# Optimization experiments

Measured on AMD Instinct MI355X. Metric: run time of the kernel, lower is better.

The kernel has to match this reference:

```python
import jax, jax.numpy as jnp
import numpy as np

B, S, H = 4, 2048, 1024
DECAY_RATE = 0.5  # MemoryModule decay: exp(-decay_rate * k), k=1 (most recent pattern)


def setup_inputs() -> dict:
    key = jax.random.key(0)
    ks = jax.random.split(key, 7)
    hidden_states = jax.random.normal(ks[0], (B, S, H), dtype=jnp.float32)
    # past attention pattern: valid row-stochastic attention probs [B, S, S]
    pa = jax.random.uniform(ks[1], (B, S, S), dtype=jnp.float32)
    past_attention = pa / pa.sum(-1, keepdims=True)
    scale = 1.0 / np.sqrt(H).astype(np.float32)
    Wq = jax.random.normal(ks[2], (H, H), dtype=jnp.float32) * scale
    Wk = jax.random.normal(ks[3], (H, H), dtype=jnp.float32) * scale
    Wv = jax.random.normal(ks[4], (H, H), dtype=jnp.float32) * scale
    Wm = jax.random.normal(ks[5], (H, H), dtype=jnp.float32) * scale
    w_gate = jax.random.normal(ks[6], (H,), dtype=jnp.float32) * scale
    return {"hidden_states": hidden_states, "past_attention": past_attention,
            "Wq": Wq, "Wk": Wk, "Wv": Wv, "Wm": Wm, "w_gate": w_gate}


def reference(hidden_states, past_attention, Wq, Wk, Wv, Wm, w_gate):
    h = hidden_states.shape[-1]
    inv_sqrt_h = 1.0 / (h ** 0.5)
    # QKV projections (hidden -> hidden)
    q = jnp.einsum('bsh,hd->bsd', hidden_states, Wq)
    k = jnp.einsum('bsh,hd->bsd', hidden_states, Wk)
    v = jnp.einsum('bsh,hd->bsd', hidden_states, Wv)
    # base attention scores QK^T / sqrt(H)
    scores = jnp.einsum('bqd,bkd->bqk', q, k) * inv_sqrt_h
    # --- memory bias ---
    # decayed history pattern (single most-recent entry, k=1)
    memory = past_attention * jnp.exp(jnp.float32(-DECAY_RATE * 1.0))  # [B,S,S]
    # per-token scalar gate from query
    gates = jax.nn.sigmoid(jnp.einsum('bsh,h->bs', q, w_gate))  # [B,S]
    memory_values = jnp.einsum('bqk,bkd->bqd', memory, v)        # memory @ V
    transformed = jnp.einsum('bsh,hd->bsd', memory_values, Wm)   # memory_transform (no bias)
    gated_memory = gates[..., None] * transformed
    memory_bias = jnp.einsum('bqd,bkd->bqk', gated_memory, k) * inv_sqrt_h
    # augmented attention
    probs = jax.nn.softmax(scores + memory_bias, axis=-1)
    context = jnp.einsum('bqk,bkd->bqd', probs, v)
    return context
```

## Files before the change

kernel.cpp:

```cpp
#include <hip/hip_runtime.h>
#include <hip/hip_bf16.h>

typedef __attribute__((ext_vector_type(4))) float f32x4;
typedef __attribute__((ext_vector_type(8))) __bf16 bf16x8;

__device__ __forceinline__ unsigned short f2bf(float f) {
    union { float f; unsigned u; } x; x.f = f;
    unsigned r = x.u + 0x7fffu + ((x.u >> 16) & 1u);
    return (unsigned short)(r >> 16);
}
__device__ __forceinline__ float bf2f(unsigned short b) {
    union { unsigned u; float f; } x; x.u = ((unsigned)b) << 16;
    return x.f;
}

__device__ __forceinline__ void gload16(const void* g, void* l) {
    __builtin_amdgcn_global_load_lds(
        (const __attribute__((address_space(1))) unsigned int*)g,
        (__attribute__((address_space(3))) unsigned int*)l,
        16, 0, 0);
}

template <int N> __device__ __forceinline__ void vm_wait();
template <> __device__ __forceinline__ void vm_wait<0>() { asm volatile("s_waitcnt vmcnt(0)" ::: "memory"); }
template <> __device__ __forceinline__ void vm_wait<2>() { asm volatile("s_waitcnt vmcnt(2)" ::: "memory"); }
template <> __device__ __forceinline__ void vm_wait<4>() { asm volatile("s_waitcnt vmcnt(4)" ::: "memory"); }

__global__ __launch_bounds__(256) void k_prep(
    const float* __restrict__ hs, const float* __restrict__ pa,
    const float* __restrict__ Wq, const float* __restrict__ Wk,
    const float* __restrict__ Wv, const float* __restrict__ Wm,
    unsigned short* __restrict__ hs_bf, unsigned short* __restrict__ pa_bf,
    unsigned short* __restrict__ WT, float decay) {
    __shared__ float tile[32][33];
    unsigned b = blockIdx.x;
    int t = threadIdx.x;
    if (b < 16384u) {
        int i = b * 256 + t;
        float4 v = reinterpret_cast<const float4*>(pa)[i];
        union { unsigned short u[4]; uint2 q; } o;
        o.u[0] = f2bf(v.x * decay); o.u[1] = f2bf(v.y * decay);
        o.u[2] = f2bf(v.z * decay); o.u[3] = f2bf(v.w * decay);
        reinterpret_cast<uint2*>(pa_bf)[i] = o.q;
    } else if (b < 24576u) {
        int i = (b - 16384u) * 256 + t;
        float4 v = reinterpret_cast<const float4*>(hs)[i];
        union { unsigned short u[4]; uint2 q; } o;
        o.u[0] = f2bf(v.x); o.u[1] = f2bf(v.y);
        o.u[2] = f2bf(v.z); o.u[3] = f2bf(v.w);
        reinterpret_cast<uint2*>(hs_bf)[i] = o.q;
    } else {
        unsigned bb = b - 24576u;
        int z = bb >> 10, rem = bb & 1023;
        int bx = rem & 31, by = rem >> 5;
        const float* src = z == 0 ? Wq : z == 1 ? Wk : z == 2 ? Wv : Wm;
        unsigned short* dst = WT + (size_t)z * 1024 * 1024;
        int lx = t & 31, ly8 = t >> 5;
        int x = bx * 32 + lx;
#pragma unroll
        for (int i = 0; i < 4; i++)
            tile[ly8 + i * 8][lx] = src[(size_t)(by * 32 + ly8 + i * 8) * 1024 + x];
        __syncthreads();
        int tx = by * 32 + lx;
#pragma unroll
        for (int i = 0; i < 4; i++)
            dst[(size_t)(bx * 32 + ly8 + i * 8) * 1024 + tx] = f2bf(tile[lx][ly8 + i * 8]);
    }
}

__global__ __launch_bounds__(256) void k_post(
    const unsigned short* __restrict__ C3, unsigned short* __restrict__ v_t,
    const float* __restrict__ wg, float* __restrict__ gates) {
    __shared__ unsigned short tile[32][33];
    unsigned b = blockIdx.x;
    int t = threadIdx.x;
    if (b < 8192u) {
        int bx = b & 31, by = (b >> 5) & 63, bz = b >> 11;
        int lx = t & 31, ly8 = t >> 5;
        int x = bx * 32 + lx;
#pragma unroll
        for (int i = 0; i < 4; i++) {
            int y = by * 32 + ly8 + i * 8;
            tile[ly8 + i * 8][lx] = C3[(size_t)(bz * 2048 + y) * 3072 + 2048 + x];
        }
        __syncthreads();
        int tx = by * 32 + lx;
#pragma unroll
        for (int i = 0; i < 4; i++) {
            int ty = bx * 32 + ly8 + i * 8;
            v_t[(size_t)bz * 1024 * 2048 + (size_t)ty * 2048 + tx] = tile[lx][ly8 + i * 8];
        }
    } else {
        unsigned bb = b - 8192u;
        int lane = t & 63;
        int row = bb * 4 + (t >> 6);
        const unsigned short* qr = C3 + (size_t)row * 3072 + lane * 16;
        uint4 a0 = *reinterpret_cast<const uint4*>(qr);
        uint4 a1 = *reinterpret_cast<const uint4*>(qr + 8);
        const float* wp = wg + lane * 16;
        float s = 0.f;
        unsigned ua[8] = {a0.x, a0.y, a0.z, a0.w, a1.x, a1.y, a1.z, a1.w};
#pragma unroll
        for (int j = 0; j < 8; j++) {
            s += bf2f((unsigned short)(ua[j] & 0xffff)) * wp[2 * j];
            s += bf2f((unsigned short)(ua[j] >> 16)) * wp[2 * j + 1];
        }
#pragma unroll
        for (int o = 1; o < 64; o <<= 1) s += __shfl_xor(s, o);
        if (lane == 0) gates[row] = 1.f / (1.f + __expf(-s));
    }
}

__global__ __launch_bounds__(256) void k_softmax(const float* __restrict__ logits,
                                                 unsigned short* __restrict__ probs) {
    __shared__ float red[8];
    size_t base = (size_t)blockIdx.x * 2048;
    const float4* src = reinterpret_cast<const float4*>(logits + base);
    int t = threadIdx.x;
    int wave = t >> 6, lane = t & 63;
    float4 v0 = src[t], v1 = src[t + 256];
    float m = fmaxf(fmaxf(fmaxf(v0.x, v0.y), fmaxf(v0.z, v0.w)),
                    fmaxf(fmaxf(v1.x, v1.y), fmaxf(v1.z, v1.w)));
#pragma unroll
    for (int o = 1; o < 64; o <<= 1) m = fmaxf(m, __shfl_xor(m, o));
    if (lane == 0) red[wave] = m;
    __syncthreads();
    m = fmaxf(fmaxf(red[0], red[1]), fmaxf(red[2], red[3]));
    float e[8];
    e[0] = __expf(v0.x - m); e[1] = __expf(v0.y - m);
    e[2] = __expf(v0.z - m); e[3] = __expf(v0.w - m);
    e[4] = __expf(v1.x - m); e[5] = __expf(v1.y - m);
    e[6] = __expf(v1.z - m); e[7] = __expf(v1.w - m);
    float s = e[0] + e[1] + e[2] + e[3] + e[4] + e[5] + e[6] + e[7];
#pragma unroll
    for (int o = 1; o < 64; o <<= 1) s += __shfl_xor(s, o);
    if (lane == 0) red[4 + wave] = s;
    __syncthreads();
    s = red[4] + red[5] + red[6] + red[7];
    float inv = 1.f / s;
    union { unsigned short u[4]; uint2 q; } o0, o1;
#pragma unroll
    for (int j = 0; j < 4; j++) o0.u[j] = f2bf(e[j] * inv);
#pragma unroll
    for (int j = 0; j < 4; j++) o1.u[j] = f2bf(e[4 + j] * inv);
    reinterpret_cast<uint2*>(probs + base)[t] = o0.q;
    reinterpret_cast<uint2*>(probs + base)[t + 256] = o1.q;
}

template <int BN>
struct Geo {
    static constexpr int WN = BN / 64;
    static constexpr int WM = 8 / WN;
    static constexpr int WROWS = 256 / WM;
    static constexpr int MF = WROWS / 16;
    static constexpr int MP = MF / 4;
    static constexpr int ASZ = 256 * 64 * 2;
    static constexpr int BSZ = BN * 64 * 2;
    static constexpr int BUFSZ = ASZ + BSZ;
};

#define GPH(BUFOFF, MB, LB, STG, VMW)                                                   \
    {                                                                                   \
        const char* aB = smem + (BUFOFF);                                               \
        const char* bB = aB + G::ASZ;                                                   \
        bf16x8 af[G::MP * 2];                                                           \
        _Pragma("unroll") for (int mm = 0; mm < G::MP; ++mm)                            \
        _Pragma("unroll") for (int kk = 0; kk < 2; ++kk) {                              \
            int rowx = wrow + ((MB) + mm) * 16 + fr;                                    \
            int slot = (kk * 4 + kq) ^ (rowx & 7);                                      \
            af[mm * 2 + kk] = *reinterpret_cast<const bf16x8*>(aB + rowx * 128 + slot * 16); \
        }                                                                               \
        if (LB) {                                                                       \
            _Pragma("unroll") for (int nn = 0; nn < 4; ++nn)                            \
            _Pragma("unroll") for (int kk = 0; kk < 2; ++kk) {                          \
                int rowx = wcol + nn * 16 + fr;                                         \
                int slot = (kk * 4 + kq) ^ (rowx & 7);                                  \
                bfrag[nn * 2 + kk] = *reinterpret_cast<const bf16x8*>(bB + rowx * 128 + slot * 16); \
            }                                                                           \
        }                                                                               \
        STG;                                                                            \
        __builtin_amdgcn_sched_barrier(0);                                              \
        VMW;                                                                            \
        __builtin_amdgcn_s_barrier();                                                   \
        asm volatile("s_waitcnt lgkmcnt(0)" ::: "memory");                              \
        __builtin_amdgcn_sched_barrier(0);                                              \
        __builtin_amdgcn_s_setprio(1);                                                  \
        _Pragma("unroll") for (int mm = 0; mm < G::MP; ++mm)                            \
        _Pragma("unroll") for (int nn = 0; nn < 4; ++nn)                                \
        _Pragma("unroll") for (int kk = 0; kk < 2; ++kk)                                \
            acc[(MB) + mm][nn] = __builtin_amdgcn_mfma_f32_16x16x32_bf16(               \
                af[mm * 2 + kk], bfrag[nn * 2 + kk], acc[(MB) + mm][nn], 0, 0, 0);      \
        __builtin_amdgcn_s_setprio(0);                                                  \
        __builtin_amdgcn_sched_barrier(0);                                              \
        __builtin_amdgcn_s_barrier();                                                   \
        __builtin_amdgcn_sched_barrier(0);                                              \
    }

template <int EPI, int BN>
__global__ __launch_bounds__(512, 2) void k_gemm8(
    const unsigned short* __restrict__ A, int ldA, long long bsA,
    const unsigned short* __restrict__ Bt, int ldB, long long bsB,
    void* __restrict__ Cv, int ldC, long long bsC,
    const unsigned short* __restrict__ Qm, int ldQ,
    const float* __restrict__ gates, float alpha, int K,
    int NX, int NY, int NB, int yf) {
    using G = Geo<BN>;
    extern __shared__ char smem[];
    const int NT = K >> 6, NI = K >> 7;

    unsigned b = blockIdx.x;
    unsigned wg = (b & 7) * (gridDim.x >> 3) + (b >> 3);
    int xT, yT, zB;
    if (yf) {
        yT = wg % NY; unsigned r2 = wg / NY;
        xT = r2 % NX; zB = (int)(r2 / NX) % NB;
    } else {
        xT = wg % NX; unsigned r2 = wg / NX;
        yT = r2 % NY; zB = (int)(r2 / NY) % NB;
    }

    const unsigned short* Ab = A + (size_t)zB * (size_t)bsA;
    const unsigned short* Bb = Bt + (size_t)zB * (size_t)bsB;

    int t = threadIdx.x, lane = t & 63, wave = t >> 6;
    int wc = wave % G::WN, wr = wave / G::WN;
    int fr = lane & 15, kq = lane >> 4;
    int wrow = wr * G::WROWS, wcol = wc * 64;
    int trow = t >> 3, csx = (t & 7) ^ (trow & 7);
    long long rowTile = (long long)yT * 256, colTile = (long long)xT * BN;

    f32x4 acc[G::MF][4];
#pragma unroll
    for (int m = 0; m < G::MF; ++m)
#pragma unroll
        for (int n = 0; n < 4; ++n) acc[m][n] = (f32x4){0.f, 0.f, 0.f, 0.f};
    bf16x8 bfrag[8];

    auto stageA = [&](int buf, int h, int tt) {
        int kt = tt < NT ? tt : NT - 1;
#pragma unroll
        for (int rr = 0; rr < 2; ++rr) {
            const unsigned short* src =
                Ab + (size_t)(rowTile + h * 128 + rr * 64 + trow) * (size_t)ldA + kt * 64 + csx * 8;
            gload16(src, smem + buf * G::BUFSZ + h * 16384 + rr * 8192 + t * 16);
        }
    };
    auto stageB = [&](int buf, int h, int tt) {
        int kt = tt < NT ? tt : NT - 1;
        if (BN == 256) {
#pragma unroll
            for (int rr = 0; rr < 2; ++rr) {
                const unsigned short* src =
                    Bb + (size_t)(colTile + h * 128 + rr * 64 + trow) * (size_t)ldB + kt * 64 + csx * 8;
                gload16(src, smem + buf * G::BUFSZ + G::ASZ + h * 16384 + rr * 8192 + t * 16);
            }
        } else {
            const unsigned short* src =
                Bb + (size_t)(colTile + h * 64 + trow) * (size_t)ldB + kt * 64 + csx * 8;
            gload16(src, smem + buf * G::BUFSZ + G::ASZ + h * 8192 + t * 16);
        }
    };

    stageA(0, 0, 0); stageA(0, 1, 0);
    stageB(0, 0, 0); stageB(0, 1, 0);
    stageB(1, 0, 1); stageB(1, 1, 1);
    __builtin_amdgcn_sched_barrier(0);
    vm_wait<0>();
    __builtin_amdgcn_s_barrier();
    __builtin_amdgcn_sched_barrier(0);

    constexpr int VMN = (BN == 256) ? 4 : 2;
    for (int i = 0; i < NI; ++i) {
        int t1 = 2 * i + 1, t2 = 2 * i + 2, t3 = 2 * i + 3;
        GPH(0,          0,         1, stageA(1, 0, t1), (void)0);
        GPH(0,          G::MP,     0, stageA(1, 1, t1), (void)0);
        GPH(0,          2 * G::MP, 0, stageB(0, 0, t2), (void)0);
        GPH(0,          3 * G::MP, 0, stageB(0, 1, t2), vm_wait<VMN>());
        GPH(G::BUFSZ,   0,         1, stageA(0, 0, t2), (void)0);
        GPH(G::BUFSZ,   G::MP,     0, stageA(0, 1, t2), (void)0);
        GPH(G::BUFSZ,   2 * G::MP, 0, stageB(1, 0, t3), (void)0);
        GPH(G::BUFSZ,   3 * G::MP, 0, stageB(1, 1, t3), vm_wait<VMN>());
    }
    vm_wait<0>();

    long long rb0 = rowTile + wrow + kq * 4;
    long long cb0 = colTile + wcol + fr;
    if (EPI == 0) {
        unsigned short* C = (unsigned short*)Cv + (size_t)zB * (size_t)bsC;
#pragma unroll
        for (int m = 0; m < G::MF; ++m)
#pragma unroll
            for (int n = 0; n < 4; ++n)
#pragma unroll
                for (int r = 0; r < 4; ++r)
                    C[(size_t)(rb0 + m * 16 + r) * (size_t)ldC + cb0 + n * 16] =
                        f2bf(acc[m][n][r] * alpha);
    } else if (EPI == 1) {
        unsigned short* C = (unsigned short*)Cv;
#pragma unroll
        for (int m = 0; m < G::MF; ++m)
#pragma unroll
            for (int r = 0; r < 4; ++r) {
                long long row = rb0 + m * 16 + r;
                float g = gates[row];
#pragma unroll
                for (int n = 0; n < 4; ++n) {
                    long long col = cb0 + n * 16;
                    float v = (bf2f(Qm[(size_t)row * (size_t)ldQ + col]) + g * acc[m][n][r]) * alpha;
                    C[(size_t)row * (size_t)ldC + col] = f2bf(v);
                }
            }
    } else {
        float* C = (float*)Cv + (size_t)zB * (size_t)bsC;
#pragma unroll
        for (int m = 0; m < G::MF; ++m)
#pragma unroll
            for (int n = 0; n < 4; ++n)
#pragma unroll
                for (int r = 0; r < 4; ++r)
                    C[(size_t)(rb0 + m * 16 + r) * (size_t)ldC + cb0 + n * 16] =
                        acc[m][n][r] * alpha;
    }
}

extern "C" void kernel_launch(void* const* d_in, const int* in_sizes, int n_in,
                              void* d_out, int out_size, void* d_ws, size_t ws_size,
                              hipStream_t stream) {
    const float* hs = (const float*)d_in[0];
    const float* pa = (const float*)d_in[1];
    const float* Wq = (const float*)d_in[2];
    const float* Wk = (const float*)d_in[3];
    const float* Wv = (const float*)d_in[4];
    const float* Wm = (const float*)d_in[5];
    const float* wg = (const float*)d_in[6];
    float* out = (float*)d_out;

    const int B = 4, S = 2048, H = 1024;
    const size_t BS = (size_t)B * S;
    const size_t BSH = BS * H;
    const size_t BSS = (size_t)B * S * S;
    const float inv_sqrt_h = 0.03125f;
    const float decay = 0.60653065971263342f;

    char* ws = (char*)d_ws;
    size_t off = 0;
    auto take = [&](size_t bytes) {
        char* p = ws + off;
        off += (bytes + 255) & ~(size_t)255;
        return p;
    };
    unsigned short* hs_bf = (unsigned short*)take(BSH * 2);
    unsigned short* WT    = (unsigned short*)take(4ull * H * H * 2);
    float* gates          = (float*)take(BS * 4);
    unsigned short* C3    = (unsigned short*)take(BS * 3 * H * 2);
    unsigned short* v_t   = (unsigned short*)take(BSH * 2);
    unsigned short* pa_bf = (unsigned short*)take(BSS * 2);
    float* logits         = (float*)take(BSS * 4);
    unsigned short* mv    = (unsigned short*)d_out;
    unsigned short* u_bf  = hs_bf;
    unsigned short* probs = pa_bf;
    unsigned short* WmT   = WT + 3ull * H * H;

    (void)hipFuncSetAttribute((const void*)k_gemm8<0, 128>, hipFuncAttributeMaxDynamicSharedMemorySize, 98304);
    (void)hipFuncSetAttribute((const void*)k_gemm8<1, 128>, hipFuncAttributeMaxDynamicSharedMemorySize, 98304);
    (void)hipFuncSetAttribute((const void*)k_gemm8<2, 128>, hipFuncAttributeMaxDynamicSharedMemorySize, 98304);
    (void)hipFuncSetAttribute((const void*)k_gemm8<2, 256>, hipFuncAttributeMaxDynamicSharedMemorySize, 131072);

    k_prep<<<dim3(28672), 256, 0, stream>>>(hs, pa, Wq, Wk, Wv, Wm, hs_bf, pa_bf, WT, decay);
    k_gemm8<0, 128><<<768, 512, 98304, stream>>>(
        hs_bf, H, 0, WT, H, 0, C3, 3 * H, 0, nullptr, 0, nullptr, 1.f, H, 24, 32, 1, 0);
    k_post<<<dim3(10240), 256, 0, stream>>>(C3, v_t, wg, gates);
    k_gemm8<0, 128><<<256, 512, 98304, stream>>>(
        pa_bf, S, (long long)S * S, v_t, S, (long long)H * S, mv, H, (long long)S * H,
        nullptr, 0, nullptr, 1.f, S, 8, 8, 4, 1);
    k_gemm8<1, 128><<<256, 512, 98304, stream>>>(
        mv, H, 0, WmT, H, 0, u_bf, H, 0, C3, 3 * H, gates, inv_sqrt_h, H, 8, 32, 1, 0);
    k_gemm8<2, 256><<<256, 512, 131072, stream>>>(
        u_bf, H, (long long)S * H, C3 + H, 3 * H, (long long)S * 3 * H,
        logits, S, (long long)S * S, nullptr, 0, nullptr, 1.f, H, 8, 8, 4, 1);
    k_softmax<<<dim3((unsigned)BS), 256, 0, stream>>>(logits, probs);
    k_gemm8<2, 128><<<256, 512, 98304, stream>>>(
        probs, S, (long long)S * S, v_t, S, (long long)H * S, out, H, (long long)S * H,
        nullptr, 0, nullptr, 1.f, S, 8, 8, 4, 1);
}
```

Measured before the change: 267.3 us.

## Switch GEMMs to 256x256 tiles with BK=32 and 4-stage LDS pipeline

Replaces the templated BN=128/256 GEMM with a single 256x256 tile kernel that uses K-step 32, a 4-buffer ring of LDS stages with three tiles of prefetch in flight, and a new swizzle for 64-byte rows. The aim is to hide global-load latency better and raise arithmetic intensity per block. The cost is halving grid sizes for several GEMMs (as few as 128 blocks on a 256-CU part), which leaves the GPU underoccupied. It also means twice as many barrier phases per unit of K.

```diff
diff --git a/kernel.cpp b/kernel.cpp
--- a/kernel.cpp
+++ b/kernel.cpp
@@ -23,8 +23,7 @@
 
 template <int N> __device__ __forceinline__ void vm_wait();
 template <> __device__ __forceinline__ void vm_wait<0>() { asm volatile("s_waitcnt vmcnt(0)" ::: "memory"); }
-template <> __device__ __forceinline__ void vm_wait<2>() { asm volatile("s_waitcnt vmcnt(2)" ::: "memory"); }
-template <> __device__ __forceinline__ void vm_wait<4>() { asm volatile("s_waitcnt vmcnt(4)" ::: "memory"); }
+template <> __device__ __forceinline__ void vm_wait<8>() { asm volatile("s_waitcnt vmcnt(8)" ::: "memory"); }
 
 __global__ __launch_bounds__(256) void k_prep(
     const float* __restrict__ hs, const float* __restrict__ pa,
@@ -147,66 +146,50 @@
     reinterpret_cast<uint2*>(probs + base)[t + 256] = o1.q;
 }
 
-template <int BN>
-struct Geo {
-    static constexpr int WN = BN / 64;
-    static constexpr int WM = 8 / WN;
-    static constexpr int WROWS = 256 / WM;
-    static constexpr int MF = WROWS / 16;
-    static constexpr int MP = MF / 4;
-    static constexpr int ASZ = 256 * 64 * 2;
-    static constexpr int BSZ = BN * 64 * 2;
-    static constexpr int BUFSZ = ASZ + BSZ;
-};
-
-#define GPH(BUFOFF, MB, LB, STG, VMW)                                                   \
-    {                                                                                   \
-        const char* aB = smem + (BUFOFF);                                               \
-        const char* bB = aB + G::ASZ;                                                   \
-        bf16x8 af[G::MP * 2];                                                           \
-        _Pragma("unroll") for (int mm = 0; mm < G::MP; ++mm)                            \
-        _Pragma("unroll") for (int kk = 0; kk < 2; ++kk) {                              \
-            int rowx = wrow + ((MB) + mm) * 16 + fr;                                    \
-            int slot = (kk * 4 + kq) ^ (rowx & 7);                                      \
-            af[mm * 2 + kk] = *reinterpret_cast<const bf16x8*>(aB + rowx * 128 + slot * 16); \
-        }                                                                               \
-        if (LB) {                                                                       \
-            _Pragma("unroll") for (int nn = 0; nn < 4; ++nn)                            \
-            _Pragma("unroll") for (int kk = 0; kk < 2; ++kk) {                          \
-                int rowx = wcol + nn * 16 + fr;                                         \
-                int slot = (kk * 4 + kq) ^ (rowx & 7);                                  \
-                bfrag[nn * 2 + kk] = *reinterpret_cast<const bf16x8*>(bB + rowx * 128 + slot * 16); \
-            }                                                                           \
-        }                                                                               \
-        STG;                                                                            \
-        __builtin_amdgcn_sched_barrier(0);                                              \
-        VMW;                                                                            \
-        __builtin_amdgcn_s_barrier();                                                   \
-        asm volatile("s_waitcnt lgkmcnt(0)" ::: "memory");                              \
-        __builtin_amdgcn_sched_barrier(0);                                              \
-        __builtin_amdgcn_s_setprio(1);                                                  \
-        _Pragma("unroll") for (int mm = 0; mm < G::MP; ++mm)                            \
-        _Pragma("unroll") for (int nn = 0; nn < 4; ++nn)                                \
-        _Pragma("unroll") for (int kk = 0; kk < 2; ++kk)                                \
-            acc[(MB) + mm][nn] = __builtin_amdgcn_mfma_f32_16x16x32_bf16(               \
-                af[mm * 2 + kk], bfrag[nn * 2 + kk], acc[(MB) + mm][nn], 0, 0, 0);      \
-        __builtin_amdgcn_s_setprio(0);                                                  \
-        __builtin_amdgcn_sched_barrier(0);                                              \
-        __builtin_amdgcn_s_barrier();                                                   \
-        __builtin_amdgcn_sched_barrier(0);                                              \
-    }
-
-template <int EPI, int BN>
-__global__ __launch_bounds__(512, 2) void k_gemm8(
+#define GPH(CUR, MB, LB, STG, VMW)                                                     \
+    {                                                                                  \
+        const char* aB = smem + (CUR) * 32768;                                         \
+        const char* bB = aB + 16384;                                                   \
+        bf16x8 af[4];                                                                  \
+        _Pragma("unroll") for (int mm = 0; mm < 4; ++mm) {                             \
+            int rowx = wrow + ((MB) + mm) * 16 + fr;                                   \
+            int slot = kq ^ ((rowx >> 1) & 3);                                         \
+            af[mm] = *reinterpret_cast<const bf16x8*>(aB + rowx * 64 + slot * 16);     \
+        }                                                                              \
+        if (LB) {                                                                      \
+            _Pragma("unroll") for (int nn = 0; nn < 4; ++nn) {                         \
+                int rowx = wcol + nn * 16 + fr;                                        \
+                int slot = kq ^ ((rowx >> 1) & 3);                                     \
+                bfrag[nn] = *reinterpret_cast<const bf16x8*>(bB + rowx * 64 + slot * 16); \
+            }                                                                          \
+        }                                                                              \
+        STG;                                                                           \
+        __builtin_amdgcn_sched_barrier(0);                                             \
+        VMW;                                                                           \
+        __builtin_amdgcn_s_barrier();                                                  \
+        asm volatile("s_waitcnt lgkmcnt(0)" ::: "memory");                             \
+        __builtin_amdgcn_sched_barrier(0);                                             \
+        __builtin_amdgcn_s_setprio(1);                                                 \
+        _Pragma("unroll") for (int mm = 0; mm < 4; ++mm)                               \
+        _Pragma("unroll") for (int nn = 0; nn < 4; ++nn)                               \
+            acc[(MB) + mm][nn] = __builtin_amdgcn_mfma_f32_16x16x32_bf16(              \
+                af[mm], bfrag[nn], acc[(MB) + mm][nn], 0, 0, 0);                       \
+        __builtin_amdgcn_s_setprio(0);                                                 \
+        __builtin_amdgcn_sched_barrier(0);                                             \
+        __builtin_amdgcn_s_barrier();                                                  \
+        __builtin_amdgcn_sched_barrier(0);                                             \
+    }
+
+template <int EPI>
+__global__ __launch_bounds__(512, 2) void k_gemm(
     const unsigned short* __restrict__ A, int ldA, long long bsA,
     const unsigned short* __restrict__ Bt, int ldB, long long bsB,
     void* __restrict__ Cv, int ldC, long long bsC,
     const unsigned short* __restrict__ Qm, int ldQ,
     const float* __restrict__ gates, float alpha, int K,
     int NX, int NY, int NB, int yf) {
-    using G = Geo<BN>;
     extern __shared__ char smem[];
-    const int NT = K >> 6, NI = K >> 7;
+    const int NT = K >> 5;
 
     unsigned b = blockIdx.x;
     unsigned wg = (b & 7) * (gridDim.x >> 3) + (b >> 3);
@@ -223,63 +206,51 @@
     const unsigned short* Bb = Bt + (size_t)zB * (size_t)bsB;
 
     int t = threadIdx.x, lane = t & 63, wave = t >> 6;
-    int wc = wave % G::WN, wr = wave / G::WN;
+    int wc = wave & 3, wr = wave >> 2;
     int fr = lane & 15, kq = lane >> 4;
-    int wrow = wr * G::WROWS, wcol = wc * 64;
-    int trow = t >> 3, csx = (t & 7) ^ (trow & 7);
-    long long rowTile = (long long)yT * 256, colTile = (long long)xT * BN;
-
-    f32x4 acc[G::MF][4];
-#pragma unroll
-    for (int m = 0; m < G::MF; ++m)
+    int wrow = wr * 128, wcol = wc * 64;
+    int trow = t >> 2;
+    int csx = (t & 3) ^ ((t >> 3) & 3);
+    long long rowTile = (long long)yT * 256, colTile = (long long)xT * 256;
+
+    f32x4 acc[8][4];
+#pragma unroll
+    for (int m = 0; m < 8; ++m)
 #pragma unroll
         for (int n = 0; n < 4; ++n) acc[m][n] = (f32x4){0.f, 0.f, 0.f, 0.f};
-    bf16x8 bfrag[8];
-
-    auto stageA = [&](int buf, int h, int tt) {
+    bf16x8 bfrag[4];
+
+    auto stageA = [&](int buf, int tt) {
         int kt = tt < NT ? tt : NT - 1;
 #pragma unroll
         for (int rr = 0; rr < 2; ++rr) {
             const unsigned short* src =
-                Ab + (size_t)(rowTile + h * 128 + rr * 64 + trow) * (size_t)ldA + kt * 64 + csx * 8;
-            gload16(src, smem + buf * G::BUFSZ + h * 16384 + rr * 8192 + t * 16);
+                Ab + (size_t)(rowTile + rr * 128 + trow) * (size_t)ldA + kt * 32 + csx * 8;
+            gload16(src, smem + buf * 32768 + rr * 8192 + t * 16);
         }
     };
-    auto stageB = [&](int buf, int h, int tt) {
+    auto stageB = [&](int buf, int tt) {
         int kt = tt < NT ? tt : NT - 1;
-        if (BN == 256) {
-#pragma unroll
-            for (int rr = 0; rr < 2; ++rr) {
-                const unsigned short* src =
-                    Bb + (size_t)(colTile + h * 128 + rr * 64 + trow) * (size_t)ldB + kt * 64 + csx * 8;
-                gload16(src, smem + buf * G::BUFSZ + G::ASZ + h * 16384 + rr * 8192 + t * 16);
-            }
-        } else {
+#pragma unroll
+        for (int rr = 0; rr < 2; ++rr) {
             const unsigned short* src =
-                Bb + (size_t)(colTile + h * 64 + trow) * (size_t)ldB + kt * 64 + csx * 8;
-            gload16(src, smem + buf * G::BUFSZ + G::ASZ + h * 8192 + t * 16);
+                Bb + (size_t)(colTile + rr * 128 + trow) * (size_t)ldB + kt * 32 + csx * 8;
+            gload16(src, smem + buf * 32768 + 16384 + rr * 8192 + t * 16);
         }
     };
 
-    stageA(0, 0, 0); stageA(0, 1, 0);
-    stageB(0, 0, 0); stageB(0, 1, 0);
-    stageB(1, 0, 1); stageB(1, 1, 1);
+    stageA(0, 0); stageB(0, 0);
+    stageA(1, 1); stageB(1, 1);
+    stageA(2, 2); stageB(2, 2);
     __builtin_amdgcn_sched_barrier(0);
-    vm_wait<0>();
+    vm_wait<8>();
     __builtin_amdgcn_s_barrier();
     __builtin_amdgcn_sched_barrier(0);
 
-    constexpr int VMN = (BN == 256) ? 4 : 2;
-    for (int i = 0; i < NI; ++i) {
-        int t1 = 2 * i + 1, t2 = 2 * i + 2, t3 = 2 * i + 3;
-        GPH(0,          0,         1, stageA(1, 0, t1), (void)0);
-        GPH(0,          G::MP,     0, stageA(1, 1, t1), (void)0);
-        GPH(0,          2 * G::MP, 0, stageB(0, 0, t2), (void)0);
-        GPH(0,          3 * G::MP, 0, stageB(0, 1, t2), vm_wait<VMN>());
-        GPH(G::BUFSZ,   0,         1, stageA(0, 0, t2), (void)0);
-        GPH(G::BUFSZ,   G::MP,     0, stageA(0, 1, t2), (void)0);
-        GPH(G::BUFSZ,   2 * G::MP, 0, stageB(1, 0, t3), (void)0);
-        GPH(G::BUFSZ,   3 * G::MP, 0, stageB(1, 1, t3), vm_wait<VMN>());
+    for (int tt = 0; tt < NT; ++tt) {
+        int cur = tt & 3, pre = (tt + 3) & 3;
+        GPH(cur, 0, 1, stageA(pre, tt + 3), (void)0);
+        GPH(cur, 4, 0, stageB(pre, tt + 3), vm_wait<8>());
     }
     vm_wait<0>();
 
@@ -288,7 +259,7 @@
     if (EPI == 0) {
         unsigned short* C = (unsigned short*)Cv + (size_t)zB * (size_t)bsC;
 #pragma unroll
-        for (int m = 0; m < G::MF; ++m)
+        for (int m = 0; m < 8; ++m)
 #pragma unroll
             for (int n = 0; n < 4; ++n)
 #pragma unroll
@@ -298,7 +269,7 @@
     } else if (EPI == 1) {
         unsigned short* C = (unsigned short*)Cv;
 #pragma unroll
-        for (int m = 0; m < G::MF; ++m)
+        for (int m = 0; m < 8; ++m)
 #pragma unroll
             for (int r = 0; r < 4; ++r) {
                 long long row = rb0 + m * 16 + r;
@@ -313,7 +284,7 @@
     } else {
         float* C = (float*)Cv + (size_t)zB * (size_t)bsC;
 #pragma unroll
-        for (int m = 0; m < G::MF; ++m)
+        for (int m = 0; m < 8; ++m)
 #pragma unroll
             for (int n = 0; n < 4; ++n)
 #pragma unroll
@@ -361,25 +332,24 @@
     unsigned short* probs = pa_bf;
     unsigned short* WmT   = WT + 3ull * H * H;
 
-    (void)hipFuncSetAttribute((const void*)k_gemm8<0, 128>, hipFuncAttributeMaxDynamicSharedMemorySize, 98304);
-    (void)hipFuncSetAttribute((const void*)k_gemm8<1, 128>, hipFuncAttributeMaxDynamicSharedMemorySize, 98304);
-    (void)hipFuncSetAttribute((const void*)k_gemm8<2, 128>, hipFuncAttributeMaxDynamicSharedMemorySize, 98304);
-    (void)hipFuncSetAttribute((const void*)k_gemm8<2, 256>, hipFuncAttributeMaxDynamicSharedMemorySize, 131072);
+    (void)hipFuncSetAttribute((const void*)k_gemm<0>, hipFuncAttributeMaxDynamicSharedMemorySize, 131072);
+    (void)hipFuncSetAttribute((const void*)k_gemm<1>, hipFuncAttributeMaxDynamicSharedMemorySize, 131072);
+    (void)hipFuncSetAttribute((const void*)k_gemm<2>, hipFuncAttributeMaxDynamicSharedMemorySize, 131072);
 
     k_prep<<<dim3(28672), 256, 0, stream>>>(hs, pa, Wq, Wk, Wv, Wm, hs_bf, pa_bf, WT, decay);
-    k_gemm8<0, 128><<<768, 512, 98304, stream>>>(
-        hs_bf, H, 0, WT, H, 0, C3, 3 * H, 0, nullptr, 0, nullptr, 1.f, H, 24, 32, 1, 0);
+    k_gemm<0><<<384, 512, 131072, stream>>>(
+        hs_bf, H, 0, WT, H, 0, C3, 3 * H, 0, nullptr, 0, nullptr, 1.f, H, 12, 32, 1, 1);
     k_post<<<dim3(10240), 256, 0, stream>>>(C3, v_t, wg, gates);
-    k_gemm8<0, 128><<<256, 512, 98304, stream>>>(
+    k_gemm<0><<<128, 512, 131072, stream>>>(
         pa_bf, S, (long long)S * S, v_t, S, (long long)H * S, mv, H, (long long)S * H,
-        nullptr, 0, nullptr, 1.f, S, 8, 8, 4, 1);
-    k_gemm8<1, 128><<<256, 512, 98304, stream>>>(
-        mv, H, 0, WmT, H, 0, u_bf, H, 0, C3, 3 * H, gates, inv_sqrt_h, H, 8, 32, 1, 0);
-    k_gemm8<2, 256><<<256, 512, 131072, stream>>>(
+        nullptr, 0, nullptr, 1.f, S, 4, 8, 4, 1);
+    k_gemm<1><<<128, 512, 131072, stream>>>(
+        mv, H, 0, WmT, H, 0, u_bf, H, 0, C3, 3 * H, gates, inv_sqrt_h, H, 4, 32, 1, 1);
+    k_gemm<2><<<256, 512, 131072, stream>>>(
         u_bf, H, (long long)S * H, C3 + H, 3 * H, (long long)S * 3 * H,
         logits, S, (long long)S * S, nullptr, 0, nullptr, 1.f, H, 8, 8, 4, 1);
     k_softmax<<<dim3((unsigned)BS), 256, 0, stream>>>(logits, probs);
-    k_gemm8<2, 128><<<256, 512, 98304, stream>>>(
+    k_gemm<2><<<128, 512, 131072, stream>>>(
         probs, S, (long long)S * S, v_t, S, (long long)H * S, out, H, (long long)S * H,
-        nullptr, 0, nullptr, 1.f, S, 8, 8, 4, 1);
-}
+        nullptr, 0, nullptr, 1.f, S, 4, 8, 4, 1);
+}
```

New measurement: 317.9 us. 18.9% more time.

## Fuse softmax exp into logits GEMM epilogue and defer normalization to PV GEMM

Applied to the files above, without the earlier changes.

The logits GEMM epilogue now computes exp of the scores, writes them directly as bf16 unnormalized probabilities, and emits per-row partial sums per column tile. A tiny kernel turns the partials into inverse row sums, and the final PV GEMM scales each output row by that inverse. This removes the fp32 logits buffer write and read (about 64MB each way) and the separate softmax pass. It drops the max subtraction, which risks overflow if scores get large, and it stores unnormalized exp values in bf16.

```diff
diff --git a/kernel.cpp b/kernel.cpp
--- a/kernel.cpp
+++ b/kernel.cpp
@@ -111,40 +111,12 @@
     }
 }
 
-__global__ __launch_bounds__(256) void k_softmax(const float* __restrict__ logits,
-                                                 unsigned short* __restrict__ probs) {
-    __shared__ float red[8];
-    size_t base = (size_t)blockIdx.x * 2048;
-    const float4* src = reinterpret_cast<const float4*>(logits + base);
-    int t = threadIdx.x;
-    int wave = t >> 6, lane = t & 63;
-    float4 v0 = src[t], v1 = src[t + 256];
-    float m = fmaxf(fmaxf(fmaxf(v0.x, v0.y), fmaxf(v0.z, v0.w)),
-                    fmaxf(fmaxf(v1.x, v1.y), fmaxf(v1.z, v1.w)));
-#pragma unroll
-    for (int o = 1; o < 64; o <<= 1) m = fmaxf(m, __shfl_xor(m, o));
-    if (lane == 0) red[wave] = m;
-    __syncthreads();
-    m = fmaxf(fmaxf(red[0], red[1]), fmaxf(red[2], red[3]));
-    float e[8];
-    e[0] = __expf(v0.x - m); e[1] = __expf(v0.y - m);
-    e[2] = __expf(v0.z - m); e[3] = __expf(v0.w - m);
-    e[4] = __expf(v1.x - m); e[5] = __expf(v1.y - m);
-    e[6] = __expf(v1.z - m); e[7] = __expf(v1.w - m);
-    float s = e[0] + e[1] + e[2] + e[3] + e[4] + e[5] + e[6] + e[7];
-#pragma unroll
-    for (int o = 1; o < 64; o <<= 1) s += __shfl_xor(s, o);
-    if (lane == 0) red[4 + wave] = s;
-    __syncthreads();
-    s = red[4] + red[5] + red[6] + red[7];
-    float inv = 1.f / s;
-    union { unsigned short u[4]; uint2 q; } o0, o1;
-#pragma unroll
-    for (int j = 0; j < 4; j++) o0.u[j] = f2bf(e[j] * inv);
-#pragma unroll
-    for (int j = 0; j < 4; j++) o1.u[j] = f2bf(e[4 + j] * inv);
-    reinterpret_cast<uint2*>(probs + base)[t] = o0.q;
-    reinterpret_cast<uint2*>(probs + base)[t + 256] = o1.q;
+__global__ __launch_bounds__(256) void k_inv(const float* __restrict__ partials,
+                                             float* __restrict__ inv_s) {
+    int r = blockIdx.x * 256 + threadIdx.x;
+    const float4* p = reinterpret_cast<const float4*>(partials + (size_t)r * 8);
+    float4 a = p[0], b = p[1];
+    inv_s[r] = 1.f / (a.x + a.y + a.z + a.w + b.x + b.y + b.z + b.w);
 }
 
 template <int BN>
@@ -310,16 +282,59 @@
                     C[(size_t)row * (size_t)ldC + col] = f2bf(v);
                 }
             }
-    } else {
+    } else if (EPI == 4) {
         float* C = (float*)Cv + (size_t)zB * (size_t)bsC;
 #pragma unroll
         for (int m = 0; m < G::MF; ++m)
 #pragma unroll
+            for (int r = 0; r < 4; ++r) {
+                long long row = rb0 + m * 16 + r;
+                float g = gates[(size_t)zB * (size_t)ldQ + row];
+#pragma unroll
+                for (int n = 0; n < 4; ++n)
+                    C[(size_t)row * (size_t)ldC + cb0 + n * 16] = acc[m][n][r] * g;
+            }
+    } else if (EPI == 5) {
+        unsigned short* C = (unsigned short*)Cv + (size_t)zB * (size_t)bsC;
+        float* partials = (float*)gates;
+        float srow[G::MF][4];
+#pragma unroll
+        for (int m = 0; m < G::MF; ++m)
+#pragma unroll
+            for (int r = 0; r < 4; ++r) srow[m][r] = 0.f;
+#pragma unroll
+        for (int m = 0; m < G::MF; ++m)
+#pragma unroll
             for (int n = 0; n < 4; ++n)
 #pragma unroll
+                for (int r = 0; r < 4; ++r) {
+                    float e = __expf(acc[m][n][r] * alpha);
+                    C[(size_t)(rb0 + m * 16 + r) * (size_t)ldC + cb0 + n * 16] = f2bf(e);
+                    srow[m][r] += e;
+                }
+#pragma unroll
+        for (int m = 0; m < G::MF; ++m)
+#pragma unroll
+            for (int r = 0; r < 4; ++r) {
+#pragma unroll
+                for (int msk = 1; msk < 16; msk <<= 1)
+                    srow[m][r] += __shfl_xor(srow[m][r], msk);
+            }
+        float* sums = (float*)smem;
+        if (fr == 0) {
+#pragma unroll
+            for (int m = 0; m < G::MF; ++m)
+#pragma unroll
                 for (int r = 0; r < 4; ++r)
-                    C[(size_t)(rb0 + m * 16 + r) * (size_t)ldC + cb0 + n * 16] =
-                        acc[m][n][r] * alpha;
+                    sums[(wrow + kq * 4 + m * 16 + r) * G::WN + wc] = srow[m][r];
+        }
+        __syncthreads();
+        if (t < 256) {
+            float s = 0.f;
+#pragma unroll
+            for (int j = 0; j < G::WN; ++j) s += sums[t * G::WN + j];
+            partials[((size_t)zB * 2048 + (size_t)rowTile + t) * 8 + xT] = s;
+        }
     }
 }
 
@@ -355,7 +370,8 @@
     unsigned short* C3    = (unsigned short*)take(BS * 3 * H * 2);
     unsigned short* v_t   = (unsigned short*)take(BSH * 2);
     unsigned short* pa_bf = (unsigned short*)take(BSS * 2);
-    float* logits         = (float*)take(BSS * 4);
+    float* partials       = (float*)take(BS * 8 * 4);
+    float* inv_s          = (float*)take(BS * 4);
     unsigned short* mv    = (unsigned short*)d_out;
     unsigned short* u_bf  = hs_bf;
     unsigned short* probs = pa_bf;
@@ -363,8 +379,8 @@
 
     (void)hipFuncSetAttribute((const void*)k_gemm8<0, 128>, hipFuncAttributeMaxDynamicSharedMemorySize, 98304);
     (void)hipFuncSetAttribute((const void*)k_gemm8<1, 128>, hipFuncAttributeMaxDynamicSharedMemorySize, 98304);
-    (void)hipFuncSetAttribute((const void*)k_gemm8<2, 128>, hipFuncAttributeMaxDynamicSharedMemorySize, 98304);
-    (void)hipFuncSetAttribute((const void*)k_gemm8<2, 256>, hipFuncAttributeMaxDynamicSharedMemorySize, 131072);
+    (void)hipFuncSetAttribute((const void*)k_gemm8<4, 128>, hipFuncAttributeMaxDynamicSharedMemorySize, 98304);
+    (void)hipFuncSetAttribute((const void*)k_gemm8<5, 256>, hipFuncAttributeMaxDynamicSharedMemorySize, 131072);
 
     k_prep<<<dim3(28672), 256, 0, stream>>>(hs, pa, Wq, Wk, Wv, Wm, hs_bf, pa_bf, WT, decay);
     k_gemm8<0, 128><<<768, 512, 98304, stream>>>(
@@ -375,11 +391,11 @@
         nullptr, 0, nullptr, 1.f, S, 8, 8, 4, 1);
     k_gemm8<1, 128><<<256, 512, 98304, stream>>>(
         mv, H, 0, WmT, H, 0, u_bf, H, 0, C3, 3 * H, gates, inv_sqrt_h, H, 8, 32, 1, 0);
-    k_gemm8<2, 256><<<256, 512, 131072, stream>>>(
+    k_gemm8<5, 256><<<256, 512, 131072, stream>>>(
         u_bf, H, (long long)S * H, C3 + H, 3 * H, (long long)S * 3 * H,
-        logits, S, (long long)S * S, nullptr, 0, nullptr, 1.f, H, 8, 8, 4, 1);
-    k_softmax<<<dim3((unsigned)BS), 256, 0, stream>>>(logits, probs);
-    k_gemm8<2, 128><<<256, 512, 98304, stream>>>(
+        probs, S, (long long)S * S, nullptr, 0, partials, 1.f, H, 8, 8, 4, 1);
+    k_inv<<<dim3(32), 256, 0, stream>>>(partials, inv_s);
+    k_gemm8<4, 128><<<256, 512, 98304, stream>>>(
         probs, S, (long long)S * S, v_t, S, (long long)H * S, out, H, (long long)S * H,
-        nullptr, 0, nullptr, 1.f, S, 8, 8, 4, 1);
-}
+        nullptr, S, inv_s, 1.f, S, 8, 8, 4, 1);
+}
```

Result: faster. 251.4 us (-5.9%).
